# Optimization experiments

Hardware: AMD Instinct MI355X
Metric: run time of the kernel (lower is better)

## Reference

```python
import jax, jax.numpy as jnp
import numpy as np

RES = 32
HEADS = 16
EMB = 1024
DIM_HEAD = EMB // HEADS
BATCH = 8
N = RES * RES
SCALE = DIM_HEAD ** -0.5


def _make_bias_idxs():
    # replicate the LeViT-style |dx|,|dy| offset indexing from __init__
    points = [(i, j) for i in range(RES) for j in range(RES)]
    offsets = {}
    idxs = []
    for p1 in points:
        for p2 in points:
            off = (abs(p1[0] - p2[0]), abs(p1[1] - p2[1]))
            if off not in offsets:
                offsets[off] = len(offsets)
            idxs.append(offsets[off])
    return np.asarray(idxs, dtype=np.int32).reshape(N, N), len(offsets)


def setup_inputs() -> dict:
    key = jax.random.key(0)
    k_x, k_qkv, k_b, k_o = jax.random.split(key, 4)
    bias_idxs, n_off = _make_bias_idxs()  # n_off == 1024 for a 32x32 grid
    return {
        "x": jax.random.normal(k_x, (BATCH, N, EMB), dtype=jnp.float32),
        "W_qkv": jax.random.normal(k_qkv, (3 * EMB, EMB), dtype=jnp.float32) * 0.02,
        "attention_biases": jax.random.normal(k_b, (HEADS, n_off), dtype=jnp.float32) * 0.02,
        "bias_idxs": jnp.asarray(bias_idxs),
        "W_out": jax.random.normal(k_o, (EMB, EMB), dtype=jnp.float32) * 0.02,
        "b_out": jnp.zeros((EMB,), dtype=jnp.float32),
    }


def reference(x, W_qkv, attention_biases, bias_idxs, W_out, b_out):
    B, n, E = x.shape
    # to_qkv: Linear(E, 3E, bias=False) -> x @ W^T
    qkv = x @ W_qkv.T  # [B, n, 3E]
    q, k, v = jnp.split(qkv, 3, axis=-1)

    def heads(t):  # b n (h d) -> b h n d
        return t.reshape(B, n, HEADS, DIM_HEAD).transpose(0, 2, 1, 3)

    q, k, v = heads(q), heads(k), heads(v)
    qk = jnp.einsum("bhnd,bhmd->bhnm", q, k) * SCALE  # [B, h, n, n]
    bias = attention_biases[:, bias_idxs]  # gather -> [h, n, n]
    qk = qk + bias[None]
    attn = jax.nn.softmax(qk, axis=-1)
    out = jnp.einsum("bhnm,bhmd->bhnd", attn, v)
    out = out.transpose(0, 2, 1, 3).reshape(B, n, E)  # b h n d -> b n (h d)
    # to_out: Linear(E, E) with bias (dropout p=0 is identity)
    return out @ W_out.T + b_out
```

## Files before the change

### kernel.cpp

```cpp
#include <hip/hip_runtime.h>

typedef __attribute__((ext_vector_type(8))) short bf16x8;
typedef __attribute__((ext_vector_type(4))) short bf16x4;
typedef __attribute__((ext_vector_type(4))) float f32x4;

#define L2E 1.44269504088896340736f
#define QSCL 0.18033688011112042f

__device__ inline unsigned short f2bf(float f) {
  union { float f; unsigned int u; } x; x.f = f;
  return (unsigned short)((x.u + 0x8000u) >> 16);
}
__device__ inline unsigned int f2bf2(float a, float b) {
  union { float f; unsigned int u; } xa, xb;
  xa.f = a; xb.f = b;
  return ((xa.u + 0x8000u) >> 16) | (((xb.u + 0x8000u) & 0xFFFF0000u));
}
__device__ inline unsigned int pk_bf16(float a, float b) {
#if __has_builtin(__builtin_amdgcn_cvt_pk_bf16_f32)
  typedef __attribute__((ext_vector_type(2))) __bf16 bfv2;
  union { bfv2 v; unsigned int u; } x;
  x.v = __builtin_amdgcn_cvt_pk_bf16_f32(a, b);
  return x.u;
#else
  return f2bf2(a, b);
#endif
}

__device__ inline void gl_lds16(const void* g, void* l) {
  __builtin_amdgcn_global_load_lds((const __attribute__((address_space(1))) void*)g,
                                   (__attribute__((address_space(3))) void*)l,
                                   16, 0, 0);
}

__device__ inline void vm_drain() {
  asm volatile("s_waitcnt vmcnt(0)" ::: "memory");
}
__device__ inline void vm_wait4() {
  asm volatile("s_waitcnt vmcnt(4)" ::: "memory");
}
__device__ inline void vm_wait3() {
  asm volatile("s_waitcnt vmcnt(3)" ::: "memory");
}

#define N4_X  2097152
#define N4_WQ 786432
#define N4_WO 262144
__global__ void cast3_kernel(const float* __restrict__ x,
                             const float* __restrict__ wq,
                             const float* __restrict__ wo,
                             unsigned short* __restrict__ xb,
                             unsigned short* __restrict__ wqb,
                             unsigned short* __restrict__ wob) {
  int i = blockIdx.x * blockDim.x + threadIdx.x;
  int st = gridDim.x * blockDim.x;
  for (; i < N4_X + N4_WQ + N4_WO; i += st) {
    const float* src; unsigned short* dst; int j;
    if (i < N4_X)            { src = x;  dst = xb;  j = i; }
    else if (i < N4_X + N4_WQ){ src = wq; dst = wqb; j = i - N4_X; }
    else                     { src = wo; dst = wob; j = i - N4_X - N4_WQ; }
    float4 v = reinterpret_cast<const float4*>(src)[j];
    ushort4 o;
    o.x = f2bf(v.x); o.y = f2bf(v.y); o.z = f2bf(v.z); o.w = f2bf(v.w);
    reinterpret_cast<ushort4*>(dst)[j] = o;
  }
}

template <int MODE>
__device__ __forceinline__ void qkv_body(
    unsigned short* lds,
    const unsigned short* __restrict__ A,
    const unsigned short* __restrict__ Bm,
    unsigned short* __restrict__ qo,
    unsigned short* __restrict__ ko,
    unsigned short* __restrict__ vo,
    int tm, int tn) {
  const int tid = threadIdx.x;
  const int w = tid >> 6, lane = tid & 63;
  const int l15 = lane & 15, quad = lane >> 4;
  const int wmb = (w >> 2) * 128;
  const int wnb = (w & 3) * 64;
  const int rl = (w << 3) + (lane >> 3);
  const int scol = ((lane & 7) ^ ((lane >> 3) & 7)) << 3;
  const int rk = l15 & 7;

  const unsigned short* Ab = A + (size_t)(tm * 256) * 1024;
  const unsigned short* Bb = Bm + (size_t)(tn * 256) * 1024;

  unsigned short* sA0 = lds;
  unsigned short* sA1 = lds + 16384;
  unsigned short* sB0 = lds + 32768;
  unsigned short* sB1 = lds + 49152;

#define STG_HALF(Gb, R0, k0, Lb)                                              \
  do {                                                                        \
    gl_lds16((Gb) + (size_t)((R0) + rl) * 1024 + (k0) + scol,                 \
             (Lb) + ((R0) + (w << 3)) * 64);                                  \
    gl_lds16((Gb) + (size_t)((R0) + 64 + rl) * 1024 + (k0) + scol,            \
             (Lb) + ((R0) + 64 + (w << 3)) * 64);                             \
  } while (0)

#define LDF(buf, row, kk) \
  (*(const bf16x8*)&(buf)[(row) * 64 + ((((kk) * 4 + quad) ^ rk) << 3)])

  STG_HALF(Ab, 0, 0, sA0);
  STG_HALF(Ab, 128, 0, sA0);
  STG_HALF(Bb, 0, 0, sB0);
  STG_HALF(Bb, 128, 0, sB0);
  STG_HALF(Bb, 0, 64, sB1);
  STG_HALF(Bb, 128, 64, sB1);

  const f32x4 fz = {0.f, 0.f, 0.f, 0.f};
  f32x4 acc[8][4];
#pragma unroll
  for (int i = 0; i < 8; i++)
#pragma unroll
    for (int j = 0; j < 4; j++) acc[i][j] = fz;

  vm_wait4();
  __syncthreads();

  for (int t = 0; t < 16; ++t) {
    unsigned short* Ac = (t & 1) ? sA1 : sA0;
    unsigned short* An = (t & 1) ? sA0 : sA1;
    unsigned short* Bc = (t & 1) ? sB1 : sB0;
    bf16x8 a0[4][2], a1[4][2], b0[2][2], b1[2][2];

#pragma unroll
    for (int mt = 0; mt < 4; mt++)
#pragma unroll
      for (int kk = 0; kk < 2; kk++)
        a0[mt][kk] = LDF(Ac, wmb + mt * 16 + l15, kk);
#pragma unroll
    for (int nt = 0; nt < 2; nt++)
#pragma unroll
      for (int kk = 0; kk < 2; kk++)
        b0[nt][kk] = LDF(Bc, wnb + nt * 16 + l15, kk);
    if (t < 15) STG_HALF(Ab, 0, (t + 1) << 6, An);
    __syncthreads();
    __builtin_amdgcn_s_setprio(1);
#pragma unroll
    for (int mt = 0; mt < 4; mt++)
#pragma unroll
      for (int nt = 0; nt < 2; nt++)
#pragma unroll
        for (int kk = 0; kk < 2; kk++)
          acc[mt][nt] = (MODE == 0)
            ? __builtin_amdgcn_mfma_f32_16x16x32_bf16(b0[nt][kk], a0[mt][kk], acc[mt][nt], 0, 0, 0)
            : __builtin_amdgcn_mfma_f32_16x16x32_bf16(a0[mt][kk], b0[nt][kk], acc[mt][nt], 0, 0, 0);
    __builtin_amdgcn_s_setprio(0);
    __syncthreads();

#pragma unroll
    for (int nt = 0; nt < 2; nt++)
#pragma unroll
      for (int kk = 0; kk < 2; kk++)
        b1[nt][kk] = LDF(Bc, wnb + (nt + 2) * 16 + l15, kk);
    if (t < 15) STG_HALF(Ab, 128, (t + 1) << 6, An);
    __syncthreads();
    __builtin_amdgcn_s_setprio(1);
#pragma unroll
    for (int mt = 0; mt < 4; mt++)
#pragma unroll
      for (int nt = 0; nt < 2; nt++)
#pragma unroll
        for (int kk = 0; kk < 2; kk++)
          acc[mt][nt + 2] = (MODE == 0)
            ? __builtin_amdgcn_mfma_f32_16x16x32_bf16(b1[nt][kk], a0[mt][kk], acc[mt][nt + 2], 0, 0, 0)
            : __builtin_amdgcn_mfma_f32_16x16x32_bf16(a0[mt][kk], b1[nt][kk], acc[mt][nt + 2], 0, 0, 0);
    __builtin_amdgcn_s_setprio(0);
    __syncthreads();

#pragma unroll
    for (int mt = 0; mt < 4; mt++)
#pragma unroll
      for (int kk = 0; kk < 2; kk++)
        a1[mt][kk] = LDF(Ac, wmb + (mt + 4) * 16 + l15, kk);
    if (t < 14) STG_HALF(Bb, 0, (t + 2) << 6, Bc);
    __syncthreads();
    __builtin_amdgcn_s_setprio(1);
#pragma unroll
    for (int mt = 0; mt < 4; mt++)
#pragma unroll
      for (int nt = 0; nt < 2; nt++)
#pragma unroll
        for (int kk = 0; kk < 2; kk++)
          acc[mt + 4][nt] = (MODE == 0)
            ? __builtin_amdgcn_mfma_f32_16x16x32_bf16(b0[nt][kk], a1[mt][kk], acc[mt + 4][nt], 0, 0, 0)
            : __builtin_amdgcn_mfma_f32_16x16x32_bf16(a1[mt][kk], b0[nt][kk], acc[mt + 4][nt], 0, 0, 0);
    __builtin_amdgcn_s_setprio(0);
    __syncthreads();

    if (t < 14) STG_HALF(Bb, 128, (t + 2) << 6, Bc);
    __syncthreads();
    __builtin_amdgcn_s_setprio(1);
#pragma unroll
    for (int mt = 0; mt < 4; mt++)
#pragma unroll
      for (int nt = 0; nt < 2; nt++)
#pragma unroll
        for (int kk = 0; kk < 2; kk++)
          acc[mt + 4][nt + 2] = (MODE == 0)
            ? __builtin_amdgcn_mfma_f32_16x16x32_bf16(b1[nt][kk], a1[mt][kk], acc[mt + 4][nt + 2], 0, 0, 0)
            : __builtin_amdgcn_mfma_f32_16x16x32_bf16(a1[mt][kk], b1[nt][kk], acc[mt + 4][nt + 2], 0, 0, 0);
    __builtin_amdgcn_s_setprio(0);
    if (t < 14) vm_wait4();
    else if (t == 14) vm_drain();
    __syncthreads();
  }
#undef STG_HALF
#undef LDF

  const int bb = tm >> 2;
  const int n0 = (tm & 3) << 8;
  const int cb = (tn & 3) << 8;
  if (MODE == 0) {
    const float scl = (tn < 4) ? QSCL : 1.0f;
    unsigned short* dst = (tn < 4) ? qo : ko;
#pragma unroll
    for (int mt = 0; mt < 8; mt++) {
      int tok = n0 + wmb + mt * 16 + l15;
#pragma unroll
      for (int nt = 0; nt < 4; nt++) {
        int c = cb + wnb + nt * 16 + quad * 4;
        int hh = c >> 6, d0 = c & 63;
        uint2 val;
        val.x = f2bf2(acc[mt][nt][0] * scl, acc[mt][nt][1] * scl);
        val.y = f2bf2(acc[mt][nt][2] * scl, acc[mt][nt][3] * scl);
        *(uint2*)&dst[(((size_t)bb * 16 + hh) * 1024 + tok) * 64 + d0] = val;
      }
    }
  } else {
#pragma unroll
    for (int mt = 0; mt < 8; mt++) {
      int tok = n0 + wmb + mt * 16 + quad * 4;
#pragma unroll
      for (int nt = 0; nt < 4; nt++) {
        int c = cb + wnb + nt * 16 + l15;
        int hh = c >> 6, dd = c & 63;
        uint2 val;
        val.x = f2bf2(acc[mt][nt][0], acc[mt][nt][1]);
        val.y = f2bf2(acc[mt][nt][2], acc[mt][nt][3]);
        *(uint2*)&vo[(((size_t)bb * 16 + hh) * 64 + dd) * 1024 + tok] = val;
      }
    }
  }
}

__global__ __launch_bounds__(512, 2) void gemm_qkv(
    const unsigned short* __restrict__ A,
    const unsigned short* __restrict__ Bm,
    unsigned short* __restrict__ qo,
    unsigned short* __restrict__ ko,
    unsigned short* __restrict__ vo) {
  __shared__ unsigned short lds[65536];
  const int id = blockIdx.x;
  const int wg = (id & 7) * 48 + (id >> 3);
  const int tm = wg / 12, tn = wg - tm * 12;
  if (tn < 8) qkv_body<0>(lds, A, Bm, qo, ko, vo, tm, tn);
  else        qkv_body<1>(lds, A, Bm, qo, ko, vo, tm, tn);
}

__global__ __launch_bounds__(256, 2) void attn_kernel(
    const unsigned short* __restrict__ Q,
    const unsigned short* __restrict__ Kg,
    const unsigned short* __restrict__ Vt,
    const float* __restrict__ biases,
    unsigned short* __restrict__ Og) {
  __shared__ unsigned short sK[2][64 * 64];
  __shared__ unsigned short sV[2][64 * 64];
  __shared__ float sBias2[32 * 63];

  const int bx = blockIdx.x;
  const int bh = bx & 127, qt = bx >> 7;
  const int h = bh & 15, b = bh >> 4;
  const int tid = threadIdx.x, w = tid >> 6, lane = tid & 63;
  const int l15 = lane & 15, quad = lane >> 4;

  const size_t bhs = (size_t)(b * 16 + h);
  const unsigned short* qbase = Q + (bhs * 1024 + (size_t)qt * 256) * 64;
  const unsigned short* kbase = Kg + bhs * 1024 * 64;
  const unsigned short* vbase = Vt + bhs * 64 * 1024;

  for (int t = tid; t < 2048; t += 256) {
    int d = t >> 6, u = t & 63;
    if (u < 63) {
      int dj = u - 31; dj = dj < 0 ? -dj : dj;
      sBias2[d * 63 + u] = biases[h * 1024 + d * 32 + dj] * L2E;
    }
  }

  const int sr0 = w * 16 + (lane >> 3);
  const int sc8 = lane & 7;
  const int sw0 = sc8 ^ (lane >> 3);

  gl_lds16(kbase + (size_t)sr0 * 64 + sw0 * 8,        &sK[0][(w * 16) * 64]);
  gl_lds16(kbase + (size_t)(sr0 + 8) * 64 + sw0 * 8,  &sK[0][(w * 16 + 8) * 64]);
  gl_lds16(vbase + (size_t)sr0 * 1024 + sw0 * 8,      &sV[0][(w * 16) * 64]);
  gl_lds16(vbase + (size_t)(sr0 + 8) * 1024 + sw0 * 8,&sV[0][(w * 16 + 8) * 64]);

  bf16x8 qf[4][2];
#pragma unroll
  for (int qb = 0; qb < 4; qb++)
#pragma unroll
    for (int kd = 0; kd < 2; kd++)
      qf[qb][kd] = *(const bf16x8*)(qbase + (w * 64 + qb * 16 + l15) * 64 + kd * 32 + quad * 8);

  const int qg0 = qt * 256 + w * 64;
  const int qtw = __builtin_amdgcn_readfirstlane(qt * 8 + w * 2);
  int cc2[2][2];
#pragma unroll
  for (int qh = 0; qh < 2; qh++)
#pragma unroll
    for (int kp = 0; kp < 2; kp++)
      cc2[qh][kp] = qh * 16 + l15 - kp * 16 - quad * 4;

  const f32x4 fz = {0.f, 0.f, 0.f, 0.f};
  f32x4 of[4][4], osum[4];
#pragma unroll
  for (int i = 0; i < 4; i++) {
    osum[i] = fz;
#pragma unroll
    for (int j = 0; j < 4; j++) of[i][j] = fz;
  }
  const bf16x4 vones = {(short)0x3F80, (short)0x3F80, (short)0x3F80, (short)0x3F80};

  int buf = 0;
  for (int j0 = 0; j0 < 1024; j0 += 64) {
    vm_drain();
    __syncthreads();
    if (j0 + 64 < 1024) {
      int nb = buf ^ 1, jn = j0 + 64;
      gl_lds16(kbase + (size_t)(jn + sr0) * 64 + sw0 * 8,       &sK[nb][(w * 16) * 64]);
      gl_lds16(kbase + (size_t)(jn + sr0 + 8) * 64 + sw0 * 8,   &sK[nb][(w * 16 + 8) * 64]);
      gl_lds16(vbase + (size_t)sr0 * 1024 + jn + sw0 * 8,       &sV[nb][(w * 16) * 64]);
      gl_lds16(vbase + (size_t)(sr0 + 8) * 1024 + jn + sw0 * 8, &sV[nb][(w * 16 + 8) * 64]);
    }
    const unsigned short* K_ = sK[buf];
    const unsigned short* V_ = sV[buf];
    const int j5 = j0 >> 5;
    const int dh = qtw - j5;
    const float* b0 = sBias2 + abs(dh) * 63 + 31;
    const float* bM = sBias2 + abs(dh - 1) * 63 + 31;
    const float* bP = sBias2 + abs(dh + 1) * 63 + 31;

#pragma unroll
    for (int kvb = 0; kvb < 4; kvb++) {
      bf16x8 kf0 = *(const bf16x8*)&K_[(kvb * 16 + l15) * 64 + ((quad ^ (l15 & 7)) << 3)];
      bf16x8 kf1 = *(const bf16x8*)&K_[(kvb * 16 + l15) * 64 + (((4 + quad) ^ (l15 & 7)) << 3)];
      bf16x4 vf[4];
#pragma unroll
      for (int nt = 0; nt < 4; nt++) {
        int d = nt * 16 + l15;
        vf[nt] = *(const bf16x4*)&V_[d * 64 + (((kvb * 2 + (quad >> 1)) ^ (l15 & 7)) << 3) + (quad & 1) * 4];
      }
      const int kp = kvb & 1;
#pragma unroll
      for (int qb = 0; qb < 4; qb++) {
        f32x4 s4 = __builtin_amdgcn_mfma_f32_16x16x32_bf16(kf0, qf[qb][0], fz, 0, 0, 0);
        s4 = __builtin_amdgcn_mfma_f32_16x16x32_bf16(kf1, qf[qb][1], s4, 0, 0, 0);
        const float* bp = (qb < 2) ? ((kvb < 2) ? b0 : bM)
                                   : ((kvb < 2) ? bP : b0);
        const float* bq = bp + cc2[qb & 1][kp];
        float p0 = __builtin_amdgcn_exp2f(s4.x + bq[0]);
        float p1 = __builtin_amdgcn_exp2f(s4.y + bq[-1]);
        float p2 = __builtin_amdgcn_exp2f(s4.z + bq[-2]);
        float p3 = __builtin_amdgcn_exp2f(s4.w + bq[-3]);
        union { unsigned int u[2]; bf16x4 v; } pk;
        pk.u[0] = pk_bf16(p0, p1);
        pk.u[1] = pk_bf16(p2, p3);
#pragma unroll
        for (int nt = 0; nt < 4; nt++)
          of[qb][nt] = __builtin_amdgcn_mfma_f32_16x16x16bf16_1k(pk.v, vf[nt], of[qb][nt], 0, 0, 0);
        osum[qb] = __builtin_amdgcn_mfma_f32_16x16x16bf16_1k(pk.v, vones, osum[qb], 0, 0, 0);
      }
    }
    buf ^= 1;
  }

  const int kvq = quad * 4;
#pragma unroll
  for (int qb = 0; qb < 4; qb++)
#pragma unroll
    for (int r = 0; r < 4; r++) {
      float inv = __builtin_amdgcn_rcpf(osum[qb][r]);
      int n = qg0 + qb * 16 + kvq + r;
      size_t orow = ((size_t)b * 1024 + n) * 1024 + h * 64;
#pragma unroll
      for (int nt = 0; nt < 4; nt++)
        Og[orow + nt * 16 + l15] = f2bf(of[qb][nt][r] * inv);
    }
}

__global__ __launch_bounds__(256, 4) void gemm_out_k(
    const unsigned short* __restrict__ A,
    const unsigned short* __restrict__ Bm,
    const float* __restrict__ bias,
    float* __restrict__ out) {
  __shared__ unsigned short sA[3][128 * 32];
  __shared__ unsigned short sB[3][64 * 32];
  const int K = 1024;
  const int tid = threadIdx.x;
  const int w = tid >> 6, lane = tid & 63;
  const int l15 = lane & 15, quad = lane >> 4;
  const int tm = blockIdx.y, tn = blockIdx.x;

  const unsigned short* Ab = A + (size_t)(tm * 128) * K;
  const unsigned short* Bb = Bm + (size_t)(tn * 64) * K;

  const int srowA = w * 32 + (lane >> 2);
  const int srowB = w * 16 + (lane >> 2);
  const int scol = (((lane & 3) ^ ((lane >> 3) & 3))) * 8;
  const int rsw = (l15 >> 1) & 3;

  const f32x4 fz = {0.f, 0.f, 0.f, 0.f};
  f32x4 acc[2][4];
#pragma unroll
  for (int i = 0; i < 2; i++)
#pragma unroll
    for (int j = 0; j < 4; j++) acc[i][j] = fz;

#define OUT_STAGE(kn, nb)                                                          \
  do {                                                                             \
    gl_lds16(Ab + (size_t)srowA * K + (kn) + scol,        &sA[nb][(w * 32) * 32]);      \
    gl_lds16(Ab + (size_t)(srowA + 16) * K + (kn) + scol, &sA[nb][(w * 32 + 16) * 32]); \
    gl_lds16(Bb + (size_t)srowB * K + (kn) + scol,        &sB[nb][(w * 16) * 32]);      \
  } while (0)

  OUT_STAGE(0, 0);
  OUT_STAGE(32, 1);

  int bi = 0;
  for (int k0 = 0; k0 < K; k0 += 32) {
    if (k0 + 64 < K) vm_wait3(); else vm_drain();
    __syncthreads();
    if (k0 + 64 < K) {
      int nb = bi + 2; if (nb >= 3) nb -= 3;
      OUT_STAGE(k0 + 64, nb);
    }
    bf16x8 af[2], bfr[4];
#pragma unroll
    for (int mt = 0; mt < 2; mt++)
      af[mt] = *(const bf16x8*)&sA[bi][(w * 32 + mt * 16 + l15) * 32 + ((quad ^ rsw) << 3)];
#pragma unroll
    for (int nt = 0; nt < 4; nt++)
      bfr[nt] = *(const bf16x8*)&sB[bi][(nt * 16 + l15) * 32 + ((quad ^ rsw) << 3)];
#pragma unroll
    for (int mt = 0; mt < 2; mt++)
#pragma unroll
      for (int nt = 0; nt < 4; nt++)
        acc[mt][nt] = __builtin_amdgcn_mfma_f32_16x16x32_bf16(af[mt], bfr[nt], acc[mt][nt], 0, 0, 0);
    bi = bi + 1; if (bi == 3) bi = 0;
  }
#undef OUT_STAGE

  const int m0 = tm * 128 + w * 32, c0 = tn * 64;
#pragma unroll
  for (int mt = 0; mt < 2; mt++)
#pragma unroll
    for (int nt = 0; nt < 4; nt++)
#pragma unroll
      for (int r = 0; r < 4; r++) {
        int m = m0 + mt * 16 + quad * 4 + r;
        int c = c0 + nt * 16 + l15;
        out[(size_t)m * 1024 + c] = acc[mt][nt][r] + bias[c];
      }
}

extern "C" void kernel_launch(void* const* d_in, const int* in_sizes, int n_in,
                              void* d_out, int out_size, void* d_ws, size_t ws_size,
                              hipStream_t stream) {
  const float* x    = (const float*)d_in[0];
  const float* Wqkv = (const float*)d_in[1];
  const float* ab   = (const float*)d_in[2];
  const float* Wout = (const float*)d_in[4];
  const float* bout = (const float*)d_in[5];
  float* out = (float*)d_out;

  char* ws = (char*)d_ws;
  unsigned short* xb  = (unsigned short*)(ws);
  unsigned short* wqb = (unsigned short*)(ws + 16777216);
  unsigned short* wob = (unsigned short*)(ws + 23068672);
  unsigned short* qw  = (unsigned short*)(ws + 25165824);
  unsigned short* kw  = (unsigned short*)(ws + 41943040);
  unsigned short* vw  = (unsigned short*)(ws + 58720256);
  unsigned short* ow  = (unsigned short*)(ws + 75497472);

  cast3_kernel<<<1536, 256, 0, stream>>>(x, Wqkv, Wout, xb, wqb, wob);
  gemm_qkv<<<384, 512, 0, stream>>>(xb, wqb, qw, kw, vw);
  attn_kernel<<<512, 256, 0, stream>>>(qw, kw, vw, ab, ow);
  gemm_out_k<<<dim3(16, 64), 256, 0, stream>>>(ow, wob, bout, out);
}
```

Measured before the change: 289.9 us.

## Prefetch A two stages ahead and replace syncthreads with raw barriers in GEMM

The GEMM mainloop now prefetches both A and B tiles two k-steps ahead, using double-buffered LDS for each, instead of prefetching A only one step ahead. The vmcnt wait depth rises to match the larger number of loads in flight. __syncthreads is replaced by a bare s_barrier with compiler memory fences, which drops the implicit full waitcnt so global-to-LDS loads can stay outstanding across barriers. This risks LDS hazards if the manual waitcnt accounting is off by one.

```diff
diff --git a/kernel.cpp b/kernel.cpp
--- a/kernel.cpp
+++ b/kernel.cpp
@@ -36,11 +36,17 @@
 __device__ inline void vm_drain() {
   asm volatile("s_waitcnt vmcnt(0)" ::: "memory");
 }
-__device__ inline void vm_wait4() {
-  asm volatile("s_waitcnt vmcnt(4)" ::: "memory");
-}
 __device__ inline void vm_wait3() {
   asm volatile("s_waitcnt vmcnt(3)" ::: "memory");
+}
+__device__ inline void vm_wait8() {
+  asm volatile("s_waitcnt vmcnt(8)" ::: "memory");
+}
+
+__device__ inline void wave_barrier() {
+  asm volatile("" ::: "memory");
+  __builtin_amdgcn_s_barrier();
+  asm volatile("" ::: "memory");
 }
 
 #define N4_X  2097152
@@ -103,12 +109,10 @@
 #define LDF(buf, row, kk) \
   (*(const bf16x8*)&(buf)[(row) * 64 + ((((kk) * 4 + quad) ^ rk) << 3)])
 
-  STG_HALF(Ab, 0, 0, sA0);
-  STG_HALF(Ab, 128, 0, sA0);
-  STG_HALF(Bb, 0, 0, sB0);
-  STG_HALF(Bb, 128, 0, sB0);
-  STG_HALF(Bb, 0, 64, sB1);
-  STG_HALF(Bb, 128, 64, sB1);
+  STG_HALF(Ab, 0, 0, sA0);  STG_HALF(Ab, 128, 0, sA0);
+  STG_HALF(Bb, 0, 0, sB0);  STG_HALF(Bb, 128, 0, sB0);
+  STG_HALF(Ab, 0, 64, sA1); STG_HALF(Ab, 128, 64, sA1);
+  STG_HALF(Bb, 0, 64, sB1); STG_HALF(Bb, 128, 64, sB1);
 
   const f32x4 fz = {0.f, 0.f, 0.f, 0.f};
   f32x4 acc[8][4];
@@ -117,13 +121,13 @@
 #pragma unroll
     for (int j = 0; j < 4; j++) acc[i][j] = fz;
 
-  vm_wait4();
-  __syncthreads();
+  vm_wait8();
+  wave_barrier();
 
   for (int t = 0; t < 16; ++t) {
     unsigned short* Ac = (t & 1) ? sA1 : sA0;
-    unsigned short* An = (t & 1) ? sA0 : sA1;
     unsigned short* Bc = (t & 1) ? sB1 : sB0;
+    const int kf = (t + 2) << 6;
     bf16x8 a0[4][2], a1[4][2], b0[2][2], b1[2][2];
 
 #pragma unroll
@@ -136,8 +140,7 @@
 #pragma unroll
       for (int kk = 0; kk < 2; kk++)
         b0[nt][kk] = LDF(Bc, wnb + nt * 16 + l15, kk);
-    if (t < 15) STG_HALF(Ab, 0, (t + 1) << 6, An);
-    __syncthreads();
+    wave_barrier();
     __builtin_amdgcn_s_setprio(1);
 #pragma unroll
     for (int mt = 0; mt < 4; mt++)
@@ -149,15 +152,14 @@
             ? __builtin_amdgcn_mfma_f32_16x16x32_bf16(b0[nt][kk], a0[mt][kk], acc[mt][nt], 0, 0, 0)
             : __builtin_amdgcn_mfma_f32_16x16x32_bf16(a0[mt][kk], b0[nt][kk], acc[mt][nt], 0, 0, 0);
     __builtin_amdgcn_s_setprio(0);
-    __syncthreads();
+    wave_barrier();
 
 #pragma unroll
     for (int nt = 0; nt < 2; nt++)
 #pragma unroll
       for (int kk = 0; kk < 2; kk++)
         b1[nt][kk] = LDF(Bc, wnb + (nt + 2) * 16 + l15, kk);
-    if (t < 15) STG_HALF(Ab, 128, (t + 1) << 6, An);
-    __syncthreads();
+    wave_barrier();
     __builtin_amdgcn_s_setprio(1);
 #pragma unroll
     for (int mt = 0; mt < 4; mt++)
@@ -169,15 +171,15 @@
             ? __builtin_amdgcn_mfma_f32_16x16x32_bf16(b1[nt][kk], a0[mt][kk], acc[mt][nt + 2], 0, 0, 0)
             : __builtin_amdgcn_mfma_f32_16x16x32_bf16(a0[mt][kk], b1[nt][kk], acc[mt][nt + 2], 0, 0, 0);
     __builtin_amdgcn_s_setprio(0);
-    __syncthreads();
+    wave_barrier();
 
 #pragma unroll
     for (int mt = 0; mt < 4; mt++)
 #pragma unroll
       for (int kk = 0; kk < 2; kk++)
         a1[mt][kk] = LDF(Ac, wmb + (mt + 4) * 16 + l15, kk);
-    if (t < 14) STG_HALF(Bb, 0, (t + 2) << 6, Bc);
-    __syncthreads();
+    if (t < 14) { STG_HALF(Bb, 0, kf, Bc); STG_HALF(Bb, 128, kf, Bc); }
+    wave_barrier();
     __builtin_amdgcn_s_setprio(1);
 #pragma unroll
     for (int mt = 0; mt < 4; mt++)
@@ -189,10 +191,10 @@
             ? __builtin_amdgcn_mfma_f32_16x16x32_bf16(b0[nt][kk], a1[mt][kk], acc[mt + 4][nt], 0, 0, 0)
             : __builtin_amdgcn_mfma_f32_16x16x32_bf16(a1[mt][kk], b0[nt][kk], acc[mt + 4][nt], 0, 0, 0);
     __builtin_amdgcn_s_setprio(0);
-    __syncthreads();
-
-    if (t < 14) STG_HALF(Bb, 128, (t + 2) << 6, Bc);
-    __syncthreads();
+    wave_barrier();
+
+    if (t < 14) { STG_HALF(Ab, 0, kf, Ac); STG_HALF(Ab, 128, kf, Ac); }
+    wave_barrier();
     __builtin_amdgcn_s_setprio(1);
 #pragma unroll
     for (int mt = 0; mt < 4; mt++)
@@ -204,9 +206,9 @@
             ? __builtin_amdgcn_mfma_f32_16x16x32_bf16(b1[nt][kk], a1[mt][kk], acc[mt + 4][nt + 2], 0, 0, 0)
             : __builtin_amdgcn_mfma_f32_16x16x32_bf16(a1[mt][kk], b1[nt][kk], acc[mt + 4][nt + 2], 0, 0, 0);
     __builtin_amdgcn_s_setprio(0);
-    if (t < 14) vm_wait4();
+    if (t < 14) vm_wait8();
     else if (t == 14) vm_drain();
-    __syncthreads();
+    wave_barrier();
   }
 #undef STG_HALF
 #undef LDF
```

After: 256.8 us. 11.4% less time.
